# Optimization experiments

Hardware: AMD Instinct MI355X
Metric: run time of the kernel (lower is better)

Reference implementation:

```python
import jax, jax.numpy as jnp
import numpy as np


def setup_inputs() -> dict:
    key = jax.random.key(0)
    k1, k2, k3 = jax.random.split(key, 3)
    B, H, S, D = 2, 16, 2048, 64
    q = jax.random.normal(k1, (B, H, S, D), dtype=jnp.float32)
    k = jax.random.normal(k2, (B, H, S, D), dtype=jnp.float32)
    v = jax.random.normal(k3, (B, H, S, D), dtype=jnp.float32)
    return {"q": q, "k": k, "v": v}


def reference(q, k, v):
    orig_dtype = q.dtype
    q = q.astype(jnp.float32)
    k = k.astype(jnp.float32)
    v = v.astype(jnp.float32)
    B, H, S, D = q.shape
    # Per-head fixed decay rate: s_h = log2(1 - 2^(-5-h))
    head_idx = jnp.arange(H, dtype=jnp.float32)
    s = jnp.log2(1.0 - jnp.exp2(-5.0 - head_idx))  # [H]
    pos = jnp.arange(S, dtype=jnp.float32)
    pos_diff = pos[:, None] - pos[None, :]  # [S, S], i - j
    # Decay matrix n[h,i,j] = 2^((i-j)*s_h), masked to causal (i >= j)
    n = jnp.exp2(pos_diff[None, :, :] * s[:, None, None])  # [H, S, S]
    causal = (pos[:, None] >= pos[None, :]).astype(jnp.float32)  # [S, S]
    n = n * causal[None, :, :]
    scale = D ** (-0.5)
    attn = jnp.einsum('bhqd,bhkd->bhqk', q * scale, k)  # [B,H,S,S]
    attn = attn * n[None]
    o = jnp.einsum('bhqk,bhkd->bhqd', attn, v)
    return o.astype(orig_dtype)
```

## Files before the change

### kernel.cpp

```cpp
#include <hip/hip_runtime.h>


#define S_LEN 2048
#define DHEAD 64
#define CHUNK 64
#define NC    32
#define BH    32
#define LDK   72

typedef float  f32x4  __attribute__((ext_vector_type(4)));
typedef short  bf16x8 __attribute__((ext_vector_type(8)));
typedef unsigned short u16x8 __attribute__((ext_vector_type(8)));
typedef unsigned short u16x4 __attribute__((ext_vector_type(4)));

static __device__ __forceinline__ unsigned short f2bf(float f) {
    unsigned int u = __float_as_uint(f);
    u += 0x7FFFu + ((u >> 16) & 1u);
    return (unsigned short)(u >> 16);
}
static __device__ __forceinline__ float bf2f(unsigned short h) {
    return __uint_as_float((unsigned int)h << 16);
}

__global__ __launch_bounds__(256)
void ret_p1(const float* __restrict__ kg, const float* __restrict__ vg,
            unsigned short* __restrict__ Ug) {
    const int c  = (int)blockIdx.x, bh = (int)blockIdx.y, h = bh & 15;
    const int tid = (int)threadIdx.x;
    const int wv = tid >> 6, ln = tid & 63, quad = ln >> 4, lnlo = ln & 15;
    const float sh = log2f(1.0f - exp2f(-5.0f - (float)h));

    __shared__ __align__(16) unsigned short Kt[CHUNK * LDK];
    __shared__ __align__(16) unsigned short Vt[CHUNK * LDK];

    const size_t cb = (size_t)bh * S_LEN * DHEAD + (size_t)c * CHUNK * DHEAD;
    const float* kp = kg + cb;
    const float* vp = vg + cb;

#pragma unroll
    for (int i = 0; i < 2; ++i) {
        const int pos0 = wv * 8 + i * 32;
        const float* pK = kp + (size_t)pos0 * DHEAD + ln;
        const float* pV = vp + (size_t)pos0 * DHEAD + ln;
        u16x8 tk, tv;
#pragma unroll
        for (int j = 0; j < 8; ++j) {
            const float w = exp2f(sh * (float)(CHUNK - pos0 - j));
            tk[j] = f2bf(pK[(size_t)j * DHEAD] * w);
            tv[j] = f2bf(pV[(size_t)j * DHEAD]);
        }
        *(u16x8*)&Kt[ln * LDK + pos0] = tk;
        *(u16x8*)&Vt[ln * LDK + pos0] = tv;
    }
    __syncthreads();

    bf16x8 aK[2];
#pragma unroll
    for (int ks = 0; ks < 2; ++ks)
        aK[ks] = *(const bf16x8*)&Kt[(wv * 16 + lnlo) * LDK + ks * 32 + quad * 8];

    unsigned short* up = Ug + ((size_t)(bh * NC + c) << 12);
#pragma unroll
    for (int nt = 0; nt < 4; ++nt) {
        f32x4 acc = (f32x4){0.f, 0.f, 0.f, 0.f};
#pragma unroll
        for (int ks = 0; ks < 2; ++ks) {
            const bf16x8 bv = *(const bf16x8*)&Vt[(nt * 16 + lnlo) * LDK + ks * 32 + quad * 8];
            acc = __builtin_amdgcn_mfma_f32_16x16x32_bf16(aK[ks], bv, acc, 0, 0, 0);
        }
        u16x4 w;
#pragma unroll
        for (int r = 0; r < 4; ++r) w[r] = f2bf(acc[r]);
        *(u16x4*)&up[(nt * 16 + lnlo) * 64 + wv * 16 + quad * 4] = w;
    }
}

__global__ __launch_bounds__(256)
void ret_p2(const unsigned short* __restrict__ Ug, unsigned short* __restrict__ Sg) {
    const int eb = (int)blockIdx.x, bh = (int)blockIdx.y, h = bh & 15;
    const float sh   = log2f(1.0f - exp2f(-5.0f - (float)h));
    const float lamC = exp2f(sh * (float)CHUNK);
    const int elem = eb * 256 + (int)threadIdx.x;

    const unsigned short* up = Ug + ((size_t)(bh * NC) << 12) + elem;
    unsigned short*       sp = Sg + ((size_t)(bh * NC) << 12) + elem;

    float S = 0.0f;
    float u = bf2f(up[0]);
    for (int c = 0; c < NC; ++c) {
        const float un = (c + 1 < NC - 1) ? bf2f(up[(size_t)(c + 1) << 12]) : 0.0f;
        sp[(size_t)c << 12] = f2bf(S);
        S = lamC * S + u;
        u = un;
    }
}

__global__ __launch_bounds__(256)
void ret_p3(const float* __restrict__ qg, const float* __restrict__ kg,
            const float* __restrict__ vg, const unsigned short* __restrict__ Sg,
            float* __restrict__ og) {
    const int c  = (int)blockIdx.x, bh = (int)blockIdx.y, h = bh & 15;
    const int tid = (int)threadIdx.x;
    const int wv = tid >> 6, ln = tid & 63, quad = ln >> 4, lnlo = ln & 15;
    const float sh    = log2f(1.0f - exp2f(-5.0f - (float)h));
    const float scale = 0.125f;

    __shared__ __align__(16) unsigned short Ks[CHUNK * LDK];
    __shared__ __align__(16) unsigned short Vt[CHUNK * LDK];
    __shared__ __align__(16) unsigned short ShL[CHUNK * LDK];

    const size_t cb = (size_t)bh * S_LEN * DHEAD + (size_t)c * CHUNK * DHEAD;
    const float* qp = qg + cb;
    const float* kp = kg + cb;
    const float* vp = vg + cb;
    float*       op = og + cb;

    {
        const int kr = tid >> 2, kc0 = (tid & 3) * 16;
        const float* p = kp + (size_t)kr * DHEAD + kc0;
        const f32x4 x0 = *(const f32x4*)(p + 0);
        const f32x4 x1 = *(const f32x4*)(p + 4);
        const f32x4 x2 = *(const f32x4*)(p + 8);
        const f32x4 x3 = *(const f32x4*)(p + 12);
        u16x8 w0, w1;
        w0[0]=f2bf(x0[0]); w0[1]=f2bf(x0[1]); w0[2]=f2bf(x0[2]); w0[3]=f2bf(x0[3]);
        w0[4]=f2bf(x1[0]); w0[5]=f2bf(x1[1]); w0[6]=f2bf(x1[2]); w0[7]=f2bf(x1[3]);
        w1[0]=f2bf(x2[0]); w1[1]=f2bf(x2[1]); w1[2]=f2bf(x2[2]); w1[3]=f2bf(x2[3]);
        w1[4]=f2bf(x3[0]); w1[5]=f2bf(x3[1]); w1[6]=f2bf(x3[2]); w1[7]=f2bf(x3[3]);
        *(u16x8*)&Ks[kr * LDK + kc0]     = w0;
        *(u16x8*)&Ks[kr * LDK + kc0 + 8] = w1;
    }
#pragma unroll
    for (int i = 0; i < 2; ++i) {
        const int pos0 = wv * 8 + i * 32;
        const float* p = vp + (size_t)pos0 * DHEAD + ln;
        u16x8 t;
#pragma unroll
        for (int j = 0; j < 8; ++j) t[j] = f2bf(p[(size_t)j * DHEAD]);
        *(u16x8*)&Vt[ln * LDK + pos0] = t;
    }
    {
        const size_t sb = ((size_t)(bh * NC + c) << 12) + (size_t)tid * 16;
        const int r = tid >> 2, ccol = (tid & 3) * 16;
        *(u16x8*)&ShL[r * LDK + ccol]     = *(const u16x8*)(Sg + sb);
        *(u16x8*)&ShL[r * LDK + ccol + 8] = *(const u16x8*)(Sg + sb + 8);
    }

    bf16x8 aQ[2];
    {
        const float* qrow = qp + (size_t)(wv * 16 + lnlo) * DHEAD;
#pragma unroll
        for (int ks = 0; ks < 2; ++ks) {
            const float* p = qrow + ks * 32 + quad * 8;
            bf16x8 a;
#pragma unroll
            for (int j = 0; j < 8; ++j) a[j] = (short)f2bf(p[j]);
            aQ[ks] = a;
        }
    }
    float rf[4];
#pragma unroll
    for (int r = 0; r < 4; ++r) rf[r] = exp2f((float)(wv * 16 + quad * 4 + r) * sh);

    __syncthreads();

    f32x4 o[4];
#pragma unroll
    for (int nt = 0; nt < 4; ++nt) {
        f32x4 a = (f32x4){0.f, 0.f, 0.f, 0.f};
#pragma unroll
        for (int ks = 0; ks < 2; ++ks) {
            const bf16x8 bs = *(const bf16x8*)&ShL[(nt * 16 + lnlo) * LDK + ks * 32 + quad * 8];
            a = __builtin_amdgcn_mfma_f32_16x16x32_bf16(aQ[ks], bs, a, 0, 0, 0);
        }
        o[nt] = a;
    }

    f32x4 acc[4];
#pragma unroll
    for (int nt = 0; nt < 4; ++nt) {
        f32x4 a = (f32x4){0.f, 0.f, 0.f, 0.f};
#pragma unroll
        for (int ks = 0; ks < 2; ++ks) {
            const bf16x8 bk = *(const bf16x8*)&Ks[(nt * 16 + lnlo) * LDK + ks * 32 + quad * 8];
            a = __builtin_amdgcn_mfma_f32_16x16x32_bf16(aQ[ks], bk, a, 0, 0, 0);
        }
        acc[nt] = a;
    }

#pragma unroll
    for (int nt = 0; nt < 4; ++nt)
#pragma unroll
        for (int r = 0; r < 4; ++r) o[nt][r] *= rf[r] * scale;

    __syncthreads();

#pragma unroll
    for (int nt = 0; nt < 4; ++nt) {
        const int jn = nt * 16 + lnlo;
        const float cf = scale * exp2f(-(float)jn * sh);
#pragma unroll
        for (int r = 0; r < 4; ++r) {
            const int ri = wv * 16 + quad * 4 + r;
            float wgt = acc[nt][r] * rf[r] * cf;
            if (ri < jn) wgt = 0.0f;
            ShL[ri * LDK + jn] = f2bf(wgt);
        }
    }
    const bf16x8 aW0 = *(const bf16x8*)&ShL[(wv * 16 + lnlo) * LDK + quad * 8];
    const bf16x8 aW1 = *(const bf16x8*)&ShL[(wv * 16 + lnlo) * LDK + 32 + quad * 8];

#pragma unroll
    for (int nt = 0; nt < 4; ++nt) {
        const bf16x8 bv0 = *(const bf16x8*)&Vt[(nt * 16 + lnlo) * LDK + quad * 8];
        const bf16x8 bv1 = *(const bf16x8*)&Vt[(nt * 16 + lnlo) * LDK + 32 + quad * 8];
        o[nt] = __builtin_amdgcn_mfma_f32_16x16x32_bf16(aW0, bv0, o[nt], 0, 0, 0);
        o[nt] = __builtin_amdgcn_mfma_f32_16x16x32_bf16(aW1, bv1, o[nt], 0, 0, 0);
    }

#pragma unroll
    for (int nt = 0; nt < 4; ++nt)
#pragma unroll
        for (int r = 0; r < 4; ++r)
            op[(size_t)(wv * 16 + quad * 4 + r) * DHEAD + nt * 16 + lnlo] = o[nt][r];
}

extern "C" void kernel_launch(void* const* d_in, const int* in_sizes, int n_in,
                              void* d_out, int out_size, void* d_ws, size_t ws_size,
                              hipStream_t stream) {
    (void)in_sizes; (void)n_in; (void)out_size; (void)ws_size;
    const float* q = (const float*)d_in[0];
    const float* k = (const float*)d_in[1];
    const float* v = (const float*)d_in[2];
    float* o  = (float*)d_out;
    unsigned short* Ug = (unsigned short*)d_ws;
    unsigned short* Sg = (unsigned short*)((char*)d_ws + (size_t)BH * NC * 4096 * 2);

    dim3 blk(256, 1, 1);
    ret_p1<<<dim3(NC - 1, BH, 1), blk, 0, stream>>>(k, v, Ug);
    ret_p2<<<dim3(16, BH, 1), blk, 0, stream>>>(Ug, Sg);
    ret_p3<<<dim3(NC, BH, 1), blk, 0, stream>>>(q, k, v, Sg, o);
}
```

Before: 104.5 us.

## Fuse chunk-state build and scan into grouped kernel with two-level prefix states

Merges the per-chunk KV outer-product kernel and the sequential scan kernel into one kernel. Each block handles a group of 4 chunks, accumulates the decayed state in registers, writes local prefix states per chunk and a group total. The output kernel then rebuilds the full inter-chunk state by adding decayed group totals to the local prefix. This removes a launch and the long serial scan pass. It also stages output through shared memory for vectorised coalesced stores and prefetches the next chunk's K/V into registers. The trade-offs are less parallelism in the first kernel (8 blocks per head instead of 31) and extra summation work per block in the output kernel.

```diff
diff --git a/kernel.cpp b/kernel.cpp
--- a/kernel.cpp
+++ b/kernel.cpp
@@ -23,91 +23,127 @@
 }
 
 __global__ __launch_bounds__(256)
-void ret_p1(const float* __restrict__ kg, const float* __restrict__ vg,
-            unsigned short* __restrict__ Ug) {
-    const int c  = (int)blockIdx.x, bh = (int)blockIdx.y, h = bh & 15;
+void ret_p12(const float* __restrict__ kg, const float* __restrict__ vg,
+             unsigned short* __restrict__ Lg, unsigned short* __restrict__ Tg) {
+    const int g  = (int)blockIdx.x, bh = (int)blockIdx.y, h = bh & 15;
     const int tid = (int)threadIdx.x;
     const int wv = tid >> 6, ln = tid & 63, quad = ln >> 4, lnlo = ln & 15;
-    const float sh = log2f(1.0f - exp2f(-5.0f - (float)h));
+    const float sh   = log2f(1.0f - exp2f(-5.0f - (float)h));
+    const float lamC = exp2f(sh * (float)CHUNK);
 
     __shared__ __align__(16) unsigned short Kt[CHUNK * LDK];
     __shared__ __align__(16) unsigned short Vt[CHUNK * LDK];
 
-    const size_t cb = (size_t)bh * S_LEN * DHEAD + (size_t)c * CHUNK * DHEAD;
-    const float* kp = kg + cb;
-    const float* vp = vg + cb;
-
-#pragma unroll
-    for (int i = 0; i < 2; ++i) {
-        const int pos0 = wv * 8 + i * 32;
-        const float* pK = kp + (size_t)pos0 * DHEAD + ln;
-        const float* pV = vp + (size_t)pos0 * DHEAD + ln;
-        u16x8 tk, tv;
-#pragma unroll
-        for (int j = 0; j < 8; ++j) {
-            const float w = exp2f(sh * (float)(CHUNK - pos0 - j));
-            tk[j] = f2bf(pK[(size_t)j * DHEAD] * w);
-            tv[j] = f2bf(pV[(size_t)j * DHEAD]);
-        }
-        *(u16x8*)&Kt[ln * LDK + pos0] = tk;
-        *(u16x8*)&Vt[ln * LDK + pos0] = tv;
-    }
-    __syncthreads();
-
-    bf16x8 aK[2];
-#pragma unroll
-    for (int ks = 0; ks < 2; ++ks)
-        aK[ks] = *(const bf16x8*)&Kt[(wv * 16 + lnlo) * LDK + ks * 32 + quad * 8];
-
-    unsigned short* up = Ug + ((size_t)(bh * NC + c) << 12);
-#pragma unroll
-    for (int nt = 0; nt < 4; ++nt) {
-        f32x4 acc = (f32x4){0.f, 0.f, 0.f, 0.f};
-#pragma unroll
-        for (int ks = 0; ks < 2; ++ks) {
-            const bf16x8 bv = *(const bf16x8*)&Vt[(nt * 16 + lnlo) * LDK + ks * 32 + quad * 8];
-            acc = __builtin_amdgcn_mfma_f32_16x16x32_bf16(aK[ks], bv, acc, 0, 0, 0);
-        }
-        u16x4 w;
-#pragma unroll
-        for (int r = 0; r < 4; ++r) w[r] = f2bf(acc[r]);
-        *(u16x4*)&up[(nt * 16 + lnlo) * 64 + wv * 16 + quad * 4] = w;
-    }
-}
-
-__global__ __launch_bounds__(256)
-void ret_p2(const unsigned short* __restrict__ Ug, unsigned short* __restrict__ Sg) {
-    const int eb = (int)blockIdx.x, bh = (int)blockIdx.y, h = bh & 15;
-    const float sh   = log2f(1.0f - exp2f(-5.0f - (float)h));
-    const float lamC = exp2f(sh * (float)CHUNK);
-    const int elem = eb * 256 + (int)threadIdx.x;
-
-    const unsigned short* up = Ug + ((size_t)(bh * NC) << 12) + elem;
-    unsigned short*       sp = Sg + ((size_t)(bh * NC) << 12) + elem;
-
-    float S = 0.0f;
-    float u = bf2f(up[0]);
-    for (int c = 0; c < NC; ++c) {
-        const float un = (c + 1 < NC - 1) ? bf2f(up[(size_t)(c + 1) << 12]) : 0.0f;
-        sp[(size_t)c << 12] = f2bf(S);
-        S = lamC * S + u;
-        u = un;
+    const size_t bb = (size_t)bh * S_LEN * DHEAD;
+
+    float rk[2][8], rv[2][8];
+    {
+        const size_t cb = bb + (size_t)(4 * g) * CHUNK * DHEAD;
+#pragma unroll
+        for (int i2 = 0; i2 < 2; ++i2) {
+            const int pos0 = wv * 8 + i2 * 32;
+            const float* pK = kg + cb + (size_t)pos0 * DHEAD + ln;
+            const float* pV = vg + cb + (size_t)pos0 * DHEAD + ln;
+#pragma unroll
+            for (int j = 0; j < 8; ++j) {
+                rk[i2][j] = pK[(size_t)j * DHEAD];
+                rv[i2][j] = pV[(size_t)j * DHEAD];
+            }
+        }
+    }
+
+    f32x4 Sreg[4];
+#pragma unroll
+    for (int nt = 0; nt < 4; ++nt) Sreg[nt] = (f32x4){0.f, 0.f, 0.f, 0.f};
+
+    for (int i = 0; i < 4; ++i) {
+        const int c = 4 * g + i;
+        if (i) {
+            unsigned short* lp = Lg + ((size_t)(bh * NC + c) << 12);
+#pragma unroll
+            for (int nt = 0; nt < 4; ++nt) {
+                u16x4 w;
+#pragma unroll
+                for (int r = 0; r < 4; ++r) w[r] = f2bf(Sreg[nt][r]);
+                *(u16x4*)&lp[(nt * 16 + lnlo) * 64 + wv * 16 + quad * 4] = w;
+            }
+        }
+        if (g == 7 && i == 3) break;
+
+#pragma unroll
+        for (int i2 = 0; i2 < 2; ++i2) {
+            const int pos0 = wv * 8 + i2 * 32;
+            u16x8 tk, tv;
+#pragma unroll
+            for (int j = 0; j < 8; ++j) {
+                const float w = exp2f(sh * (float)(CHUNK - pos0 - j));
+                tk[j] = f2bf(rk[i2][j] * w);
+                tv[j] = f2bf(rv[i2][j]);
+            }
+            *(u16x8*)&Kt[ln * LDK + pos0] = tk;
+            *(u16x8*)&Vt[ln * LDK + pos0] = tv;
+        }
+        __syncthreads();
+
+        if (i < 3 && !(g == 7 && i == 2)) {
+            const size_t cb = bb + (size_t)(c + 1) * CHUNK * DHEAD;
+#pragma unroll
+            for (int i2 = 0; i2 < 2; ++i2) {
+                const int pos0 = wv * 8 + i2 * 32;
+                const float* pK = kg + cb + (size_t)pos0 * DHEAD + ln;
+                const float* pV = vg + cb + (size_t)pos0 * DHEAD + ln;
+#pragma unroll
+                for (int j = 0; j < 8; ++j) {
+                    rk[i2][j] = pK[(size_t)j * DHEAD];
+                    rv[i2][j] = pV[(size_t)j * DHEAD];
+                }
+            }
+        }
+
+        bf16x8 aK[2];
+#pragma unroll
+        for (int ks = 0; ks < 2; ++ks)
+            aK[ks] = *(const bf16x8*)&Kt[(wv * 16 + lnlo) * LDK + ks * 32 + quad * 8];
+#pragma unroll
+        for (int nt = 0; nt < 4; ++nt) {
+            f32x4 acc = (f32x4){0.f, 0.f, 0.f, 0.f};
+#pragma unroll
+            for (int ks = 0; ks < 2; ++ks) {
+                const bf16x8 bv = *(const bf16x8*)&Vt[(nt * 16 + lnlo) * LDK + ks * 32 + quad * 8];
+                acc = __builtin_amdgcn_mfma_f32_16x16x32_bf16(aK[ks], bv, acc, 0, 0, 0);
+            }
+#pragma unroll
+            for (int r = 0; r < 4; ++r) Sreg[nt][r] = lamC * Sreg[nt][r] + acc[r];
+        }
+        __syncthreads();
+    }
+
+    if (g < 7) {
+        unsigned short* tp = Tg + ((size_t)(bh * 8 + g) << 12);
+#pragma unroll
+        for (int nt = 0; nt < 4; ++nt) {
+            u16x4 w;
+#pragma unroll
+            for (int r = 0; r < 4; ++r) w[r] = f2bf(Sreg[nt][r]);
+            *(u16x4*)&tp[(nt * 16 + lnlo) * 64 + wv * 16 + quad * 4] = w;
+        }
     }
 }
 
 __global__ __launch_bounds__(256)
 void ret_p3(const float* __restrict__ qg, const float* __restrict__ kg,
-            const float* __restrict__ vg, const unsigned short* __restrict__ Sg,
-            float* __restrict__ og) {
+            const float* __restrict__ vg, const unsigned short* __restrict__ Lg,
+            const unsigned short* __restrict__ Tg, float* __restrict__ og) {
     const int c  = (int)blockIdx.x, bh = (int)blockIdx.y, h = bh & 15;
     const int tid = (int)threadIdx.x;
     const int wv = tid >> 6, ln = tid & 63, quad = ln >> 4, lnlo = ln & 15;
     const float sh    = log2f(1.0f - exp2f(-5.0f - (float)h));
     const float scale = 0.125f;
 
-    __shared__ __align__(16) unsigned short Ks[CHUNK * LDK];
-    __shared__ __align__(16) unsigned short Vt[CHUNK * LDK];
-    __shared__ __align__(16) unsigned short ShL[CHUNK * LDK];
+    __shared__ __align__(16) unsigned short smem[3 * CHUNK * LDK];
+    unsigned short* const Ks  = smem;
+    unsigned short* const Vt  = smem + CHUNK * LDK;
+    unsigned short* const ShL = smem + 2 * CHUNK * LDK;
 
     const size_t cb = (size_t)bh * S_LEN * DHEAD + (size_t)c * CHUNK * DHEAD;
     const float* qp = qg + cb;
@@ -140,10 +176,32 @@
         *(u16x8*)&Vt[ln * LDK + pos0] = t;
     }
     {
-        const size_t sb = ((size_t)(bh * NC + c) << 12) + (size_t)tid * 16;
+        const int g = c >> 2;
         const int r = tid >> 2, ccol = (tid & 3) * 16;
-        *(u16x8*)&ShL[r * LDK + ccol]     = *(const u16x8*)(Sg + sb);
-        *(u16x8*)&ShL[r * LDK + ccol + 8] = *(const u16x8*)(Sg + sb + 8);
+        float accS[16];
+        if (c & 3) {
+            const unsigned short* lp = Lg + ((size_t)(bh * NC + c) << 12) + (size_t)tid * 16;
+            const u16x8 a0 = *(const u16x8*)lp;
+            const u16x8 a1 = *(const u16x8*)(lp + 8);
+#pragma unroll
+            for (int j = 0; j < 8; ++j) { accS[j] = bf2f(a0[j]); accS[8 + j] = bf2f(a1[j]); }
+        } else {
+#pragma unroll
+            for (int j = 0; j < 16; ++j) accS[j] = 0.f;
+        }
+        for (int gp = 0; gp < g; ++gp) {
+            const float w = exp2f(sh * (float)(CHUNK * (c - 4 * gp - 4)));
+            const unsigned short* tp = Tg + ((size_t)(bh * 8 + gp) << 12) + (size_t)tid * 16;
+            const u16x8 t0 = *(const u16x8*)tp;
+            const u16x8 t1 = *(const u16x8*)(tp + 8);
+#pragma unroll
+            for (int j = 0; j < 8; ++j) { accS[j] += w * bf2f(t0[j]); accS[8 + j] += w * bf2f(t1[j]); }
+        }
+        u16x8 w0, w1;
+#pragma unroll
+        for (int j = 0; j < 8; ++j) { w0[j] = f2bf(accS[j]); w1[j] = f2bf(accS[8 + j]); }
+        *(u16x8*)&ShL[r * LDK + ccol]     = w0;
+        *(u16x8*)&ShL[r * LDK + ccol + 8] = w1;
     }
 
     bf16x8 aQ[2];
@@ -218,11 +276,22 @@
         o[nt] = __builtin_amdgcn_mfma_f32_16x16x32_bf16(aW1, bv1, o[nt], 0, 0, 0);
     }
 
+    __syncthreads();
+    float* const Of = (float*)smem;
 #pragma unroll
     for (int nt = 0; nt < 4; ++nt)
 #pragma unroll
         for (int r = 0; r < 4; ++r)
-            op[(size_t)(wv * 16 + quad * 4 + r) * DHEAD + nt * 16 + lnlo] = o[nt][r];
+            Of[(wv * 16 + quad * 4 + r) * 68 + nt * 16 + lnlo] = o[nt][r];
+    {
+        const int row = tid >> 2, col0 = (tid & 3) * 16;
+        const float* src = &Of[row * 68 + col0];
+        float* dst = op + (size_t)row * DHEAD + col0;
+        *(f32x4*)(dst + 0)  = *(const f32x4*)(src + 0);
+        *(f32x4*)(dst + 4)  = *(const f32x4*)(src + 4);
+        *(f32x4*)(dst + 8)  = *(const f32x4*)(src + 8);
+        *(f32x4*)(dst + 12) = *(const f32x4*)(src + 12);
+    }
 }
 
 extern "C" void kernel_launch(void* const* d_in, const int* in_sizes, int n_in,
@@ -233,11 +302,10 @@
     const float* k = (const float*)d_in[1];
     const float* v = (const float*)d_in[2];
     float* o  = (float*)d_out;
-    unsigned short* Ug = (unsigned short*)d_ws;
-    unsigned short* Sg = (unsigned short*)((char*)d_ws + (size_t)BH * NC * 4096 * 2);
+    unsigned short* Lg = (unsigned short*)d_ws;
+    unsigned short* Tg = (unsigned short*)((char*)d_ws + (16u << 20));
 
     dim3 blk(256, 1, 1);
-    ret_p1<<<dim3(NC - 1, BH, 1), blk, 0, stream>>>(k, v, Ug);
-    ret_p2<<<dim3(16, BH, 1), blk, 0, stream>>>(Ug, Sg);
-    ret_p3<<<dim3(NC, BH, 1), blk, 0, stream>>>(q, k, v, Sg, o);
-}
+    ret_p12<<<dim3(8, BH, 1), blk, 0, stream>>>(k, v, Lg, Tg);
+    ret_p3<<<dim3(NC, BH, 1), blk, 0, stream>>>(q, k, v, Lg, Tg, o);
+}
```

After: 105.6 us. No clear change (+1.1%).

## Stage output through LDS for vectorized stores and drop a barrier via separate weight buffer

Applied to the files above, without the earlier changes.

The third kernel now writes the masked decay-weighted scores into a dedicated LDS buffer instead of overwriting the state tile. That removes one __syncthreads and lets the inter-chunk state MFMA run after the weight write. The output is staged through LDS with a padded stride so each thread writes 16 contiguous floats as f32x4 stores, replacing strided scalar global stores. The scan kernel is fully unrolled with a simpler load pattern. The cost is more LDS per block (four tiles) and an extra barrier before the output staging.

```diff
diff --git a/kernel.cpp b/kernel.cpp
--- a/kernel.cpp
+++ b/kernel.cpp
@@ -86,12 +86,13 @@
     unsigned short*       sp = Sg + ((size_t)(bh * NC) << 12) + elem;
 
     float S = 0.0f;
-    float u = bf2f(up[0]);
+#pragma unroll
     for (int c = 0; c < NC; ++c) {
-        const float un = (c + 1 < NC - 1) ? bf2f(up[(size_t)(c + 1) << 12]) : 0.0f;
         sp[(size_t)c << 12] = f2bf(S);
-        S = lamC * S + u;
-        u = un;
+        if (c < NC - 1) {
+            const float u = bf2f(up[(size_t)c << 12]);
+            S = lamC * S + u;
+        }
     }
 }
 
@@ -105,9 +106,11 @@
     const float sh    = log2f(1.0f - exp2f(-5.0f - (float)h));
     const float scale = 0.125f;
 
-    __shared__ __align__(16) unsigned short Ks[CHUNK * LDK];
-    __shared__ __align__(16) unsigned short Vt[CHUNK * LDK];
-    __shared__ __align__(16) unsigned short ShL[CHUNK * LDK];
+    __shared__ __align__(16) unsigned short smem[4 * CHUNK * LDK];
+    unsigned short* const Ks  = smem;
+    unsigned short* const Vt  = smem + CHUNK * LDK;
+    unsigned short* const ShL = smem + 2 * CHUNK * LDK;
+    unsigned short* const Ws  = smem + 3 * CHUNK * LDK;
 
     const size_t cb = (size_t)bh * S_LEN * DHEAD + (size_t)c * CHUNK * DHEAD;
     const float* qp = qg + cb;
@@ -164,18 +167,6 @@
 
     __syncthreads();
 
-    f32x4 o[4];
-#pragma unroll
-    for (int nt = 0; nt < 4; ++nt) {
-        f32x4 a = (f32x4){0.f, 0.f, 0.f, 0.f};
-#pragma unroll
-        for (int ks = 0; ks < 2; ++ks) {
-            const bf16x8 bs = *(const bf16x8*)&ShL[(nt * 16 + lnlo) * LDK + ks * 32 + quad * 8];
-            a = __builtin_amdgcn_mfma_f32_16x16x32_bf16(aQ[ks], bs, a, 0, 0, 0);
-        }
-        o[nt] = a;
-    }
-
     f32x4 acc[4];
 #pragma unroll
     for (int nt = 0; nt < 4; ++nt) {
@@ -187,13 +178,6 @@
         }
         acc[nt] = a;
     }
-
-#pragma unroll
-    for (int nt = 0; nt < 4; ++nt)
-#pragma unroll
-        for (int r = 0; r < 4; ++r) o[nt][r] *= rf[r] * scale;
-
-    __syncthreads();
 
 #pragma unroll
     for (int nt = 0; nt < 4; ++nt) {
@@ -204,11 +188,28 @@
             const int ri = wv * 16 + quad * 4 + r;
             float wgt = acc[nt][r] * rf[r] * cf;
             if (ri < jn) wgt = 0.0f;
-            ShL[ri * LDK + jn] = f2bf(wgt);
-        }
-    }
-    const bf16x8 aW0 = *(const bf16x8*)&ShL[(wv * 16 + lnlo) * LDK + quad * 8];
-    const bf16x8 aW1 = *(const bf16x8*)&ShL[(wv * 16 + lnlo) * LDK + 32 + quad * 8];
+            Ws[ri * LDK + jn] = f2bf(wgt);
+        }
+    }
+
+    f32x4 o[4];
+#pragma unroll
+    for (int nt = 0; nt < 4; ++nt) {
+        f32x4 a = (f32x4){0.f, 0.f, 0.f, 0.f};
+#pragma unroll
+        for (int ks = 0; ks < 2; ++ks) {
+            const bf16x8 bs = *(const bf16x8*)&ShL[(nt * 16 + lnlo) * LDK + ks * 32 + quad * 8];
+            a = __builtin_amdgcn_mfma_f32_16x16x32_bf16(aQ[ks], bs, a, 0, 0, 0);
+        }
+        o[nt] = a;
+    }
+#pragma unroll
+    for (int nt = 0; nt < 4; ++nt)
+#pragma unroll
+        for (int r = 0; r < 4; ++r) o[nt][r] *= rf[r] * scale;
+
+    const bf16x8 aW0 = *(const bf16x8*)&Ws[(wv * 16 + lnlo) * LDK + quad * 8];
+    const bf16x8 aW1 = *(const bf16x8*)&Ws[(wv * 16 + lnlo) * LDK + 32 + quad * 8];
 
 #pragma unroll
     for (int nt = 0; nt < 4; ++nt) {
@@ -218,11 +219,22 @@
         o[nt] = __builtin_amdgcn_mfma_f32_16x16x32_bf16(aW1, bv1, o[nt], 0, 0, 0);
     }
 
+    __syncthreads();
+    float* const Of = (float*)smem;
 #pragma unroll
     for (int nt = 0; nt < 4; ++nt)
 #pragma unroll
         for (int r = 0; r < 4; ++r)
-            op[(size_t)(wv * 16 + quad * 4 + r) * DHEAD + nt * 16 + lnlo] = o[nt][r];
+            Of[(wv * 16 + quad * 4 + r) * 68 + nt * 16 + lnlo] = o[nt][r];
+    {
+        const int row = tid >> 2, col0 = (tid & 3) * 16;
+        const float* src = &Of[row * 68 + col0];
+        float* dst = op + (size_t)row * DHEAD + col0;
+        *(f32x4*)(dst + 0)  = *(const f32x4*)(src + 0);
+        *(f32x4*)(dst + 4)  = *(const f32x4*)(src + 4);
+        *(f32x4*)(dst + 8)  = *(const f32x4*)(src + 8);
+        *(f32x4*)(dst + 12) = *(const f32x4*)(src + 12);
+    }
 }
 
 extern "C" void kernel_launch(void* const* d_in, const int* in_sizes, int n_in,
```

New measurement: 107.5 us. +2.9%, slower.
